# Kernel optimization log

Hardware: AMD Instinct MI355X
Metric: run time of the kernel (lower is better)

## Reference

```python
import jax, jax.numpy as jnp
import numpy as np

D_MODEL = 1024
N_HEADS = 16
D_K = D_MODEL // N_HEADS


def setup_inputs() -> dict:
    key = jax.random.key(0)
    k1, k2, k3 = jax.random.split(key, 3)
    x = jax.random.normal(k1, (4, 2048, D_MODEL), dtype=jnp.float32)
    # torch nn.Linear(d, 3d, bias=False): y = x @ W.T ; we store W.T directly as (in, out)
    w_qkv = jax.random.normal(k2, (D_MODEL, 3 * D_MODEL), dtype=jnp.float32) * (1.0 / np.sqrt(D_MODEL))
    w_out = jax.random.normal(k3, (D_MODEL, D_MODEL), dtype=jnp.float32) * (1.0 / np.sqrt(D_MODEL))
    return {"x": x, "w_qkv": w_qkv, "w_out": w_out}


def reference(x, w_qkv, w_out):
    B, T, D = x.shape
    qkv = jnp.einsum('btd,de->bte', x, w_qkv)  # (B,T,3D)
    q, k, v = jnp.split(qkv, 3, axis=-1)
    # split heads -> (B,H,T,d_k)
    def split_heads(t):
        return t.reshape(B, T, N_HEADS, D_K).transpose(0, 2, 1, 3)
    q, k, v = split_heads(q), split_heads(k), split_heads(v)
    scale = 1.0 / np.sqrt(D_K).astype(np.float32)
    scores = jnp.einsum('bhqd,bhkd->bhqk', q, k) * scale  # (B,H,T,T)
    causal = jnp.triu(jnp.full((T, T), -jnp.inf, dtype=scores.dtype), k=1)
    scores = scores + causal[None, None]
    weights = jax.nn.softmax(scores, axis=-1)
    attn = jnp.einsum('bhqk,bhkd->bhqd', weights, v)
    attn = attn.transpose(0, 2, 1, 3).reshape(B, T, D)
    return jnp.einsum('btd,de->bte', attn, w_out)
```

## Files before the change

### kernel.cpp

```cpp
#include <hip/hip_runtime.h>
#include <hip/hip_bf16.h>

typedef short short8 __attribute__((ext_vector_type(8)));
typedef float f32x4 __attribute__((ext_vector_type(4)));
typedef float f32x16 __attribute__((ext_vector_type(16)));

#define MFMA16(a, b, c) __builtin_amdgcn_mfma_f32_16x16x32_bf16((a), (b), (c), 0, 0, 0)
#define MFMA32(a, b, c) __builtin_amdgcn_mfma_f32_32x32x16_bf16((a), (b), (c), 0, 0, 0)

#define GLOAD16(gp, lp)                                                    \
    __builtin_amdgcn_global_load_lds(                                      \
        (const __attribute__((address_space(1))) unsigned int*)(gp),       \
        (__attribute__((address_space(3))) unsigned int*)(lp), 16, 0, 0)

__device__ __forceinline__ unsigned short f2b(float x) {
    unsigned int u = __float_as_uint(x);
    unsigned int r = u + 0x7FFFu + ((u >> 16) & 1u);
    return (unsigned short)(r >> 16);
}

#if __has_builtin(__builtin_amdgcn_cvt_pk_bf16_f32)
__device__ __forceinline__ unsigned pack2(float a, float b) {
    auto v = __builtin_amdgcn_cvt_pk_bf16_f32(a, b);
    unsigned u;
    __builtin_memcpy(&u, &v, 4);
    return u;
}
#else
__device__ __forceinline__ unsigned pack2(float a, float b) {
    return (unsigned)f2b(a) | ((unsigned)f2b(b) << 16);
}
#endif

__global__ __launch_bounds__(256) void cast4_kernel(const float* __restrict__ in,
                                                    unsigned short* __restrict__ out,
                                                    int n4) {
    int i = blockIdx.x * 256 + threadIdx.x;
    if (i < n4) {
        float4 v = ((const float4*)in)[i];
        ushort4 o;
        o.x = f2b(v.x); o.y = f2b(v.y); o.z = f2b(v.z); o.w = f2b(v.w);
        ((ushort4*)out)[i] = o;
    }
}

__global__ __launch_bounds__(256) void transpose_cast_f32(const float* __restrict__ in,
                                                          unsigned short* __restrict__ out,
                                                          int K, int N) {
    __shared__ unsigned short Ls[64 * 66];
    const int k0 = blockIdx.y * 64, n0 = blockIdx.x * 64;
    const int tid = threadIdx.x;
    const int krow = tid >> 4, nc4 = (tid & 15) * 4;
#pragma unroll
    for (int p = 0; p < 4; p++) {
        float4 v = *(const float4*)(in + (size_t)(k0 + krow + p * 16) * N + n0 + nc4);
        unsigned* d32 = (unsigned*)(Ls + (krow + p * 16) * 66 + nc4);
        d32[0] = pack2(v.x, v.y);
        d32[1] = pack2(v.z, v.w);
    }
    __syncthreads();
    const int n = tid >> 3, kc = (tid & 7) * 8;
#pragma unroll
    for (int p = 0; p < 2; p++) {
        int nn = n + p * 32;
        unsigned short w[8];
#pragma unroll
        for (int j = 0; j < 8; j++) w[j] = Ls[(kc + j) * 66 + nn];
        *(short8*)(out + (size_t)(n0 + nn) * K + k0 + kc) = *(short8*)w;
    }
}

__global__ __launch_bounds__(256) void gemm_qkv(const unsigned short* __restrict__ A,
                                                const unsigned short* __restrict__ Bt,
                                                unsigned short* __restrict__ Qb,
                                                unsigned short* __restrict__ Kb,
                                                unsigned short* __restrict__ Vt) {
    const int K = 1024, lda = 1024;
    __shared__ unsigned short smem[8192];
    unsigned short* As = smem;
    unsigned short* Bs = smem + 4096;

    const int tid  = threadIdx.x;
    const int wave = tid >> 6;
    const int lane = tid & 63;
    const int l32  = lane & 31;
    const int hi   = lane >> 5;
    const int m0 = blockIdx.y * 128;
    const int n0 = blockIdx.x * 128;
    const int wm = (wave >> 1) * 64;
    const int wn = (wave & 1) * 64;

    const int srow = lane >> 2;
    const int scol = (((lane & 3) ^ ((lane >> 3) & 3)) * 8);
    const int fsw  = ((l32 >> 1) & 3);

    const unsigned short* Ag0 = A  + (size_t)(m0 + wave * 32 + srow)      * lda + scol;
    const unsigned short* Ag1 = A  + (size_t)(m0 + wave * 32 + 16 + srow) * lda + scol;
    const unsigned short* Bg0 = Bt + (size_t)(n0 + wave * 32 + srow)      * K + scol;
    const unsigned short* Bg1 = Bt + (size_t)(n0 + wave * 32 + 16 + srow) * K + scol;
    unsigned short* Al0 = As + (wave * 2 + 0) * 512;
    unsigned short* Al1 = As + (wave * 2 + 1) * 512;
    unsigned short* Bl0 = Bs + (wave * 2 + 0) * 512;
    unsigned short* Bl1 = Bs + (wave * 2 + 1) * 512;

    f32x16 acc[2][2] = {};

    for (int k0 = 0; k0 < K; k0 += 32) {
        __syncthreads();
        GLOAD16(Ag0 + k0, Al0);
        GLOAD16(Ag1 + k0, Al1);
        GLOAD16(Bg0 + k0, Bl0);
        GLOAD16(Bg1 + k0, Bl1);
        __syncthreads();

        short8 af[2][2], bf[2][2];
#pragma unroll
        for (int i = 0; i < 2; i++) {
            const int row = wm + i * 32 + l32;
#pragma unroll
            for (int ks = 0; ks < 2; ks++)
                af[i][ks] = *(const short8*)(As + row * 32 + ((ks * 2 + hi) ^ fsw) * 8);
        }
#pragma unroll
        for (int j = 0; j < 2; j++) {
            const int row = wn + j * 32 + l32;
#pragma unroll
            for (int ks = 0; ks < 2; ks++)
                bf[j][ks] = *(const short8*)(Bs + row * 32 + ((ks * 2 + hi) ^ fsw) * 8);
        }
#pragma unroll
        for (int ks = 0; ks < 2; ks++)
#pragma unroll
            for (int i = 0; i < 2; i++)
#pragma unroll
                for (int j = 0; j < 2; j++)
                    acc[i][j] = MFMA32(af[i][ks], bf[j][ks], acc[i][j]);
    }

    if (n0 < 2048) {
        unsigned short* outp = (n0 < 1024) ? Qb : Kb;
        const int cb = (n0 < 1024) ? n0 : n0 - 1024;
        const float QS = (n0 < 1024) ? 0.125f * 1.44269504f : 1.0f;
#pragma unroll
        for (int i = 0; i < 2; i++)
#pragma unroll
            for (int j = 0; j < 2; j++)
#pragma unroll
                for (int r = 0; r < 16; r++) {
                    int row = m0 + wm + i * 32 + (r & 3) + 8 * (r >> 2) + 4 * hi;
                    int col = cb + wn + j * 32 + l32;
                    outp[(size_t)row * 1024 + col] = f2b(acc[i][j][r] * QS);
                }
    } else {
        const int b = m0 >> 11;
        const int t0b = m0 & 2047;
        const int hbase = (n0 - 2048) >> 6;
        __syncthreads();
#pragma unroll
        for (int p = 0; p < 2; p++) {
            if ((wave & 1) == p) {
#pragma unroll
                for (int i = 0; i < 2; i++)
#pragma unroll
                    for (int j = 0; j < 2; j++) {
                        const int c = j * 32 + l32;
#pragma unroll
                        for (int rg = 0; rg < 4; rg++) {
                            const int rowbase = wm + i * 32 + rg * 8 + 4 * hi;
                            uint2 v;
                            v.x = pack2(acc[i][j][4 * rg + 0], acc[i][j][4 * rg + 1]);
                            v.y = pack2(acc[i][j][4 * rg + 2], acc[i][j][4 * rg + 3]);
                            const int w = c * 64 + ((rowbase >> 1) ^ (4 * (c & 7)));
                            *(uint2*)(smem + 2 * w) = v;
                        }
                    }
            }
            __syncthreads();
#pragma unroll
            for (int it = 0; it < 4; it++) {
                const int id = it * 256 + tid;
                const int c = id >> 4, rg = id & 15;
                const int w = c * 64 + ((rg * 4) ^ (4 * (c & 7)));
                short8 v = *(const short8*)(smem + 2 * w);
                const int h = hbase + p;
                *(short8*)(Vt + ((size_t)((b * 16 + h) * 64 + c)) * 2048 + t0b + rg * 8) = v;
            }
            __syncthreads();
        }
    }
}

__global__ __launch_bounds__(256) void gemm_out(const unsigned short* __restrict__ A,
                                                const unsigned short* __restrict__ Bt,
                                                float* __restrict__ C) {
    const int K = 1024, lda = 1024;
    __shared__ unsigned short As[64 * 32];
    __shared__ unsigned short Bs[128 * 32];

    const int tid  = threadIdx.x;
    const int wave = tid >> 6;
    const int lane = tid & 63;
    const int l32  = lane & 31;
    const int hi   = lane >> 5;
    const int m0 = blockIdx.y * 64;
    const int n0 = blockIdx.x * 128;
    const int wm = (wave >> 1) * 32;
    const int wn = (wave & 1) * 64;

    const int srow = lane >> 2;
    const int scol = (((lane & 3) ^ ((lane >> 3) & 3)) * 8);
    const int fsw  = ((l32 >> 1) & 3);

    const unsigned short* Ag  = A  + (size_t)(m0 + wave * 16 + srow) * lda + scol;
    const unsigned short* Bg0 = Bt + (size_t)(n0 + wave * 32 + srow)      * K + scol;
    const unsigned short* Bg1 = Bt + (size_t)(n0 + wave * 32 + 16 + srow) * K + scol;
    unsigned short* Al  = As + wave * 512;
    unsigned short* Bl0 = Bs + (wave * 2 + 0) * 512;
    unsigned short* Bl1 = Bs + (wave * 2 + 1) * 512;

    f32x16 acc[2] = {};

    for (int k0 = 0; k0 < K; k0 += 32) {
        __syncthreads();
        GLOAD16(Ag + k0, Al);
        GLOAD16(Bg0 + k0, Bl0);
        GLOAD16(Bg1 + k0, Bl1);
        __syncthreads();

        short8 af[2], bf[2][2];
        {
            const int row = wm + l32;
#pragma unroll
            for (int ks = 0; ks < 2; ks++)
                af[ks] = *(const short8*)(As + row * 32 + ((ks * 2 + hi) ^ fsw) * 8);
        }
#pragma unroll
        for (int j = 0; j < 2; j++) {
            const int row = wn + j * 32 + l32;
#pragma unroll
            for (int ks = 0; ks < 2; ks++)
                bf[j][ks] = *(const short8*)(Bs + row * 32 + ((ks * 2 + hi) ^ fsw) * 8);
        }
#pragma unroll
        for (int ks = 0; ks < 2; ks++)
#pragma unroll
            for (int j = 0; j < 2; j++)
                acc[j] = MFMA32(af[ks], bf[j][ks], acc[j]);
    }

#pragma unroll
    for (int j = 0; j < 2; j++)
#pragma unroll
        for (int r = 0; r < 16; r++) {
            int row = m0 + wm + (r & 3) + 8 * (r >> 2) + 4 * hi;
            int col = n0 + wn + j * 32 + l32;
            C[(size_t)row * 1024 + col] = acc[j][r];
        }
}

__global__ __launch_bounds__(256) void attention_kernel(const unsigned short* Qb,
                                                        const unsigned short* Kb,
                                                        const unsigned short* Vt,
                                                        unsigned short* attn) {
    const int T = 2048;
    const int bi = blockIdx.x;
    const int qb = 31 - (bi >> 6);
    const int hb = bi & 63;
    const int b = hb >> 4, h = hb & 15;
    const int qb0 = qb * 64;
    const int tid = threadIdx.x, wave = tid >> 6, lane = tid & 63;
    const int l16 = lane & 15, quad = lane >> 4;
    const int qw0 = qb0 + wave * 16;

    const unsigned short* Qp  = Qb + (size_t)b * T * 1024 + h * 64;
    const unsigned short* Kp  = Kb + (size_t)b * T * 1024 + h * 64;
    const unsigned short* Vbh = Vt + ((size_t)(b * 16 + h) * 64) * 2048;

    __shared__ unsigned short Ks[2][64 * 32];
    __shared__ unsigned short Vts[2][64 * 32];
    __shared__ unsigned short Ps[4][16 * 40];
    unsigned short* Psw = Ps[wave];

    short8 qf[2];
#pragma unroll
    for (int kd = 0; kd < 2; kd++)
        qf[kd] = *(const short8*)(Qp + (size_t)(qw0 + l16) * 1024 + kd * 32 + quad * 8);

    f32x4 o[4] = {};
    float l_acc = 0.f;

    const int srow = lane >> 2;
    const int scol = (((lane & 3) ^ ((lane >> 3) & 3)) * 8);
    const int sw8  = ((l16 >> 1) & 3) * 8;
    const size_t ktstep = (wave < 2) ? (size_t)64 * 1024 : (size_t)64;
    const size_t cstep  = (wave < 2) ? (size_t)16 * 1024 : (size_t)16 * T;
    const unsigned short* g0 = (wave < 2)
            ? Kp + (size_t)srow * 1024 + wave * 32 + scol
            : Vbh + (size_t)srow * T + (wave - 2) * 32 + scol;
    unsigned short* l0 = (wave < 2) ? Ks[wave] : Vts[wave - 2];

    for (int kt = 0; kt <= qb; kt++) {
        const int tk0 = kt * 64;
        const unsigned short* g = g0 + (size_t)kt * ktstep;
        __syncthreads();
#pragma unroll
        for (int c = 0; c < 4; c++) GLOAD16(g + c * cstep, l0 + c * 512);
        __syncthreads();

#pragma unroll
        for (int th = 0; th < 2; th++) {
            if (tk0 + th * 32 > qw0 + 15) continue;

            f32x4 s[2];
            bool act[2];
#pragma unroll
            for (int mi = 0; mi < 2; mi++) {
                const int t0 = tk0 + (th * 2 + mi) * 16;
                act[mi] = (t0 <= qw0 + 15);
                s[mi] = (f32x4){0.f, 0.f, 0.f, 0.f};
                if (act[mi]) {
                    const int row = (th * 2 + mi) * 16 + l16;
                    short8 kf0 = *(const short8*)(Ks[0] + row * 32 + (quad * 8 ^ sw8));
                    short8 kf1 = *(const short8*)(Ks[1] + row * 32 + (quad * 8 ^ sw8));
                    s[mi] = MFMA16(kf0, qf[0], s[mi]);
                    s[mi] = MFMA16(kf1, qf[1], s[mi]);
                }
            }
#pragma unroll
            for (int mi = 0; mi < 2; mi++) {
                const int t0 = tk0 + (th * 2 + mi) * 16;
                unsigned pk0 = 0, pk1 = 0;
                if (act[mi]) {
                    const bool full = (t0 + 15) <= qw0;
                    float p[4];
#pragma unroll
                    for (int r = 0; r < 4; r++) {
                        float e = __builtin_amdgcn_exp2f(s[mi][r]);
                        if (!full)
                            e = (t0 + quad * 4 + r <= qw0 + l16) ? e : 0.f;
                        p[r] = e;
                    }
                    l_acc += (p[0] + p[1]) + (p[2] + p[3]);
                    pk0 = pack2(p[0], p[1]);
                    pk1 = pack2(p[2], p[3]);
                }
                uint2 pr; pr.x = pk0; pr.y = pk1;
                *(uint2*)(Psw + l16 * 40 + mi * 16 + quad * 4) = pr;
            }
            short8 pf = *(const short8*)(Psw + l16 * 40 + quad * 8);
#pragma unroll
            for (int dt = 0; dt < 4; dt++) {
                short8 vf = *(const short8*)(Vts[th] + (dt * 16 + l16) * 32 + (quad * 8 ^ sw8));
                o[dt] = MFMA16(vf, pf, o[dt]);
            }
        }
    }

    float l = l_acc;
    l += __shfl_xor(l, 16);
    l += __shfl_xor(l, 32);
    const float rl = 1.f / l;
    const int q = qw0 + l16;
#pragma unroll
    for (int dt = 0; dt < 4; dt++) {
        ushort4 wv;
        wv.x = f2b(o[dt][0] * rl);
        wv.y = f2b(o[dt][1] * rl);
        wv.z = f2b(o[dt][2] * rl);
        wv.w = f2b(o[dt][3] * rl);
        *(ushort4*)(attn + (size_t)(b * T + q) * 1024 + h * 64 + dt * 16 + quad * 4) = wv;
    }
}

extern "C" void kernel_launch(void* const* d_in, const int* in_sizes, int n_in,
                              void* d_out, int out_size, void* d_ws, size_t ws_size,
                              hipStream_t stream) {
    const float* x     = (const float*)d_in[0];
    const float* w_qkv = (const float*)d_in[1];
    const float* w_out = (const float*)d_in[2];
    float* out = (float*)d_out;

    const int M = 8192, D = 1024, E = 3072;
    const size_t MB = 1048576;

    char* ws = (char*)d_ws;
    unsigned short* xb    = (unsigned short*)ws;
    unsigned short* wqkvT = (unsigned short*)(ws + 16 * MB);
    unsigned short* woutT = (unsigned short*)(ws + 22 * MB);
    unsigned short* Qb    = (unsigned short*)(ws + 24 * MB);
    unsigned short* Kb    = (unsigned short*)(ws + 40 * MB);
    unsigned short* Vt    = (unsigned short*)(ws + 56 * MB);

    cast4_kernel<<<M * D / 4 / 256, 256, 0, stream>>>(x, xb, M * D / 4);
    transpose_cast_f32<<<dim3(E / 64, D / 64), 256, 0, stream>>>(w_qkv, wqkvT, D, E);
    transpose_cast_f32<<<dim3(D / 64, D / 64), 256, 0, stream>>>(w_out, woutT, D, D);

    gemm_qkv<<<dim3(E / 128, M / 128), 256, 0, stream>>>(xb, wqkvT, Qb, Kb, Vt);

    attention_kernel<<<dim3(2048), 256, 0, stream>>>(Qb, Kb, Vt, Qb);

    gemm_out<<<dim3(D / 128, M / 64), 256, 0, stream>>>(Qb, woutT, out);
}
```

Before: 267.0 us.

## Rewrite QKV GEMM with 256x256 tiles, double-buffered LDS pipeline and block swizzle

```diff
diff --git a/kernel.cpp b/kernel.cpp
--- a/kernel.cpp
+++ b/kernel.cpp
@@ -70,122 +70,175 @@
     }
 }
 
-__global__ __launch_bounds__(256) void gemm_qkv(const unsigned short* __restrict__ A,
-                                                const unsigned short* __restrict__ Bt,
-                                                unsigned short* __restrict__ Qb,
-                                                unsigned short* __restrict__ Kb,
-                                                unsigned short* __restrict__ Vt) {
-    const int K = 1024, lda = 1024;
-    __shared__ unsigned short smem[8192];
-    unsigned short* As = smem;
-    unsigned short* Bs = smem + 4096;
+__global__ __launch_bounds__(512, 2) void gemm_qkv(const unsigned short* __restrict__ A,
+                                                   const unsigned short* __restrict__ Bt,
+                                                   unsigned short* __restrict__ Qb,
+                                                   unsigned short* __restrict__ Kb,
+                                                   unsigned short* __restrict__ Vt) {
+    __shared__ __align__(16) unsigned short smem[65536];
 
     const int tid  = threadIdx.x;
     const int wave = tid >> 6;
     const int lane = tid & 63;
     const int l32  = lane & 31;
     const int hi   = lane >> 5;
-    const int m0 = blockIdx.y * 128;
-    const int n0 = blockIdx.x * 128;
-    const int wm = (wave >> 1) * 64;
-    const int wn = (wave & 1) * 64;
-
-    const int srow = lane >> 2;
-    const int scol = (((lane & 3) ^ ((lane >> 3) & 3)) * 8);
-    const int fsw  = ((l32 >> 1) & 3);
-
-    const unsigned short* Ag0 = A  + (size_t)(m0 + wave * 32 + srow)      * lda + scol;
-    const unsigned short* Ag1 = A  + (size_t)(m0 + wave * 32 + 16 + srow) * lda + scol;
-    const unsigned short* Bg0 = Bt + (size_t)(n0 + wave * 32 + srow)      * K + scol;
-    const unsigned short* Bg1 = Bt + (size_t)(n0 + wave * 32 + 16 + srow) * K + scol;
-    unsigned short* Al0 = As + (wave * 2 + 0) * 512;
-    unsigned short* Al1 = As + (wave * 2 + 1) * 512;
-    unsigned short* Bl0 = Bs + (wave * 2 + 0) * 512;
-    unsigned short* Bl1 = Bs + (wave * 2 + 1) * 512;
-
-    f32x16 acc[2][2] = {};
-
-    for (int k0 = 0; k0 < K; k0 += 32) {
-        __syncthreads();
-        GLOAD16(Ag0 + k0, Al0);
-        GLOAD16(Ag1 + k0, Al1);
-        GLOAD16(Bg0 + k0, Bl0);
-        GLOAD16(Bg1 + k0, Bl1);
-        __syncthreads();
-
-        short8 af[2][2], bf[2][2];
-#pragma unroll
-        for (int i = 0; i < 2; i++) {
-            const int row = wm + i * 32 + l32;
-#pragma unroll
-            for (int ks = 0; ks < 2; ks++)
-                af[i][ks] = *(const short8*)(As + row * 32 + ((ks * 2 + hi) ^ fsw) * 8);
-        }
-#pragma unroll
-        for (int j = 0; j < 2; j++) {
-            const int row = wn + j * 32 + l32;
-#pragma unroll
-            for (int ks = 0; ks < 2; ks++)
-                bf[j][ks] = *(const short8*)(Bs + row * 32 + ((ks * 2 + hi) ^ fsw) * 8);
-        }
-#pragma unroll
-        for (int ks = 0; ks < 2; ks++)
-#pragma unroll
-            for (int i = 0; i < 2; i++)
-#pragma unroll
-                for (int j = 0; j < 2; j++)
-                    acc[i][j] = MFMA32(af[i][ks], bf[j][ks], acc[i][j]);
-    }
+    const int wr   = wave >> 2;
+    const int wc   = wave & 3;
+
+    const int bid = blockIdx.x;
+    const int sid = (bid & 7) * 48 + (bid >> 3);
+    const int bx  = sid % 12;
+    const int by  = sid / 12;
+    const int m0 = by * 256;
+    const int n0 = bx * 256;
+
+    const int srow = tid >> 3;
+    const int cswz = (((tid & 7) ^ ((tid >> 3) & 7)) * 8);
+    const unsigned short* gA = A  + (size_t)(m0 + srow) * 1024 + cswz;
+    const unsigned short* gB = Bt + (size_t)(n0 + srow) * 1024 + cswz;
+
+#define STAGE_A(buf, h, kt) do {                                              \
+        const unsigned short* _g = gA + (size_t)((h) * 128) * 1024 + (kt) * 64; \
+        unsigned short* _l = smem + (buf) * 16384 + (h) * 8192 + wave * 512;  \
+        GLOAD16(_g, _l);                                                      \
+        GLOAD16(_g + 65536, _l + 4096);                                       \
+    } while (0)
+#define STAGE_B(buf, h, kt) do {                                              \
+        const unsigned short* _g = gB + (size_t)((h) * 128) * 1024 + (kt) * 64; \
+        unsigned short* _l = smem + 32768 + (buf) * 16384 + (h) * 8192 + wave * 512; \
+        GLOAD16(_g, _l);                                                      \
+        GLOAD16(_g + 65536, _l + 4096);                                       \
+    } while (0)
+
+    const int sw7  = l32 & 7;
+    const int aoff = (wr * 128 + l32) * 64;
+    const int boff = (wc * 64 + l32) * 64;
+
+    f32x16 acc[4][2] = {};
+
+    STAGE_A(0, 0, 0); STAGE_A(0, 1, 0); STAGE_B(0, 0, 0); STAGE_B(0, 1, 0);
+    STAGE_B(1, 0, 1); STAGE_B(1, 1, 1); STAGE_A(1, 0, 1);
+    asm volatile("s_waitcnt vmcnt(6)" ::: "memory");
+    __builtin_amdgcn_s_barrier();
+
+#pragma unroll
+    for (int t = 0; t < 16; ++t) {
+        const int b = t & 1;
+        const unsigned short* Ab = smem + b * 16384;
+        const unsigned short* Bb = smem + 32768 + b * 16384;
+
+        short8 afLo[2][4], afHi[2][4], bf0[4], bf1[4];
+
+#pragma unroll
+        for (int rf = 0; rf < 2; ++rf)
+#pragma unroll
+            for (int ks = 0; ks < 4; ++ks)
+                afLo[rf][ks] = *(const short8*)(Ab + aoff + rf * 2048 + (((ks * 2 + hi) ^ sw7) * 8));
+#pragma unroll
+        for (int ks = 0; ks < 4; ++ks)
+            bf0[ks] = *(const short8*)(Bb + boff + (((ks * 2 + hi) ^ sw7) * 8));
+        if (t + 1 < 16) STAGE_A(b ^ 1, 1, t + 1);
+        __builtin_amdgcn_s_barrier();
+        asm volatile("s_waitcnt lgkmcnt(0)" ::: "memory");
+        __builtin_amdgcn_s_setprio(1);
+#pragma unroll
+        for (int ks = 0; ks < 4; ++ks) {
+            acc[0][0] = MFMA32(afLo[0][ks], bf0[ks], acc[0][0]);
+            acc[1][0] = MFMA32(afLo[1][ks], bf0[ks], acc[1][0]);
+        }
+        __builtin_amdgcn_s_setprio(0);
+        __builtin_amdgcn_s_barrier();
+
+#pragma unroll
+        for (int ks = 0; ks < 4; ++ks)
+            bf1[ks] = *(const short8*)(Bb + boff + 2048 + (((ks * 2 + hi) ^ sw7) * 8));
+        __builtin_amdgcn_s_barrier();
+        asm volatile("s_waitcnt lgkmcnt(0)" ::: "memory");
+        __builtin_amdgcn_s_setprio(1);
+#pragma unroll
+        for (int ks = 0; ks < 4; ++ks) {
+            acc[0][1] = MFMA32(afLo[0][ks], bf1[ks], acc[0][1]);
+            acc[1][1] = MFMA32(afLo[1][ks], bf1[ks], acc[1][1]);
+        }
+        __builtin_amdgcn_s_setprio(0);
+        __builtin_amdgcn_s_barrier();
+
+#pragma unroll
+        for (int rf = 0; rf < 2; ++rf)
+#pragma unroll
+            for (int ks = 0; ks < 4; ++ks)
+                afHi[rf][ks] = *(const short8*)(Ab + aoff + (2 + rf) * 2048 + (((ks * 2 + hi) ^ sw7) * 8));
+        if (t + 2 < 16) { STAGE_B(b, 0, t + 2); STAGE_B(b, 1, t + 2); }
+        __builtin_amdgcn_s_barrier();
+        asm volatile("s_waitcnt lgkmcnt(0)" ::: "memory");
+        __builtin_amdgcn_s_setprio(1);
+#pragma unroll
+        for (int ks = 0; ks < 4; ++ks) {
+            acc[2][0] = MFMA32(afHi[0][ks], bf0[ks], acc[2][0]);
+            acc[3][0] = MFMA32(afHi[1][ks], bf0[ks], acc[3][0]);
+        }
+        __builtin_amdgcn_s_setprio(0);
+        __builtin_amdgcn_s_barrier();
+
+        if (t + 2 < 16) {
+            STAGE_A(b, 0, t + 2);
+            asm volatile("s_waitcnt vmcnt(6)" ::: "memory");
+        } else {
+            asm volatile("s_waitcnt vmcnt(0)" ::: "memory");
+        }
+        __builtin_amdgcn_s_barrier();
+        __builtin_amdgcn_s_setprio(1);
+#pragma unroll
+        for (int ks = 0; ks < 4; ++ks) {
+            acc[2][1] = MFMA32(afHi[0][ks], bf1[ks], acc[2][1]);
+            acc[3][1] = MFMA32(afHi[1][ks], bf1[ks], acc[3][1]);
+        }
+        __builtin_amdgcn_s_setprio(0);
+        __builtin_amdgcn_s_barrier();
+    }
+#undef STAGE_A
+#undef STAGE_B
 
     if (n0 < 2048) {
         unsigned short* outp = (n0 < 1024) ? Qb : Kb;
         const int cb = (n0 < 1024) ? n0 : n0 - 1024;
         const float QS = (n0 < 1024) ? 0.125f * 1.44269504f : 1.0f;
 #pragma unroll
-        for (int i = 0; i < 2; i++)
-#pragma unroll
-            for (int j = 0; j < 2; j++)
-#pragma unroll
-                for (int r = 0; r < 16; r++) {
-                    int row = m0 + wm + i * 32 + (r & 3) + 8 * (r >> 2) + 4 * hi;
-                    int col = cb + wn + j * 32 + l32;
-                    outp[(size_t)row * 1024 + col] = f2b(acc[i][j][r] * QS);
+        for (int rf = 0; rf < 4; ++rf)
+#pragma unroll
+            for (int cf = 0; cf < 2; ++cf)
+#pragma unroll
+                for (int r = 0; r < 16; ++r) {
+                    int row = m0 + wr * 128 + rf * 32 + (r & 3) + 8 * (r >> 2) + 4 * hi;
+                    int col = cb + wc * 64 + cf * 32 + l32;
+                    outp[(size_t)row * 1024 + col] = f2b(acc[rf][cf][r] * QS);
                 }
     } else {
-        const int b = m0 >> 11;
-        const int t0b = m0 & 2047;
+        const int bb = m0 >> 11, t0b = m0 & 2047;
         const int hbase = (n0 - 2048) >> 6;
+        unsigned short* reg = smem + wc * 16384;
+#pragma unroll
+        for (int rf = 0; rf < 4; ++rf)
+#pragma unroll
+            for (int cf = 0; cf < 2; ++cf)
+#pragma unroll
+                for (int rg = 0; rg < 4; ++rg) {
+                    const int tl = wr * 128 + rf * 32 + rg * 8 + 4 * hi;
+                    const int d  = cf * 32 + l32;
+                    const int w  = d * 128 + ((tl >> 1) ^ (4 * (d & 7)));
+                    uint2 v;
+                    v.x = pack2(acc[rf][cf][4 * rg + 0], acc[rf][cf][4 * rg + 1]);
+                    v.y = pack2(acc[rf][cf][4 * rg + 2], acc[rf][cf][4 * rg + 3]);
+                    *(uint2*)(reg + 2 * w) = v;
+                }
         __syncthreads();
 #pragma unroll
-        for (int p = 0; p < 2; p++) {
-            if ((wave & 1) == p) {
-#pragma unroll
-                for (int i = 0; i < 2; i++)
-#pragma unroll
-                    for (int j = 0; j < 2; j++) {
-                        const int c = j * 32 + l32;
-#pragma unroll
-                        for (int rg = 0; rg < 4; rg++) {
-                            const int rowbase = wm + i * 32 + rg * 8 + 4 * hi;
-                            uint2 v;
-                            v.x = pack2(acc[i][j][4 * rg + 0], acc[i][j][4 * rg + 1]);
-                            v.y = pack2(acc[i][j][4 * rg + 2], acc[i][j][4 * rg + 3]);
-                            const int w = c * 64 + ((rowbase >> 1) ^ (4 * (c & 7)));
-                            *(uint2*)(smem + 2 * w) = v;
-                        }
-                    }
-            }
-            __syncthreads();
-#pragma unroll
-            for (int it = 0; it < 4; it++) {
-                const int id = it * 256 + tid;
-                const int c = id >> 4, rg = id & 15;
-                const int w = c * 64 + ((rg * 4) ^ (4 * (c & 7)));
-                short8 v = *(const short8*)(smem + 2 * w);
-                const int h = hbase + p;
-                *(short8*)(Vt + ((size_t)((b * 16 + h) * 64 + c)) * 2048 + t0b + rg * 8) = v;
-            }
-            __syncthreads();
+        for (int it = 0; it < 16; ++it) {
+            const int id = it * 512 + tid;
+            const int hh = id >> 11, d = (id >> 5) & 63, k = id & 31;
+            short8 v = *(const short8*)(smem + hh * 16384 +
+                                        2 * (d * 128 + ((4 * k) ^ (4 * (d & 7)))));
+            *(short8*)(Vt + ((size_t)((bb * 16 + hbase + hh) * 64 + d)) * 2048 + t0b + k * 8) = v;
         }
     }
 }
@@ -395,7 +448,7 @@
     transpose_cast_f32<<<dim3(E / 64, D / 64), 256, 0, stream>>>(w_qkv, wqkvT, D, E);
     transpose_cast_f32<<<dim3(D / 64, D / 64), 256, 0, stream>>>(w_out, woutT, D, D);
 
-    gemm_qkv<<<dim3(E / 128, M / 128), 256, 0, stream>>>(xb, wqkvT, Qb, Kb, Vt);
+    gemm_qkv<<<dim3(384), 512, 0, stream>>>(xb, wqkvT, Qb, Kb, Vt);
 
     attention_kernel<<<dim3(2048), 256, 0, stream>>>(Qb, Kb, Vt, Qb);
 
```

Result: faster. 257.3 us (-3.6%).
